# Kernel tuning notes

Measured on AMD Instinct MI355X. Metric: run time of the kernel, lower is better.

Reference implementation:

```python
import jax, jax.numpy as jnp
import numpy as np

B, L, A, D = 4, 512, 8, 256
H = 256  # hidden_dim
O = 256  # output_dim


def setup_inputs() -> dict:
    key = jax.random.key(0)
    ks = jax.random.split(key, 12)
    s = 0.05
    return {
        "x": jax.random.normal(ks[0], (B, L, A, D), dtype=jnp.float32),
        "conv_w": jax.random.normal(ks[1], (H, D), dtype=jnp.float32) * s,
        "conv_b": jax.random.normal(ks[2], (H,), dtype=jnp.float32) * s,
        "theta_w": jax.random.normal(ks[3], (H, H), dtype=jnp.float32) * s,
        "theta_b": jax.random.normal(ks[4], (H,), dtype=jnp.float32) * s,
        "phi_w": jax.random.normal(ks[5], (H, H), dtype=jnp.float32) * s,
        "phi_b": jax.random.normal(ks[6], (H,), dtype=jnp.float32) * s,
        "g_w": jax.random.normal(ks[7], (H, H), dtype=jnp.float32) * s,
        "g_b": jax.random.normal(ks[8], (H,), dtype=jnp.float32) * s,
        "f_w": jax.random.normal(ks[9], (O, H), dtype=jnp.float32) * s,
        "f_b": jax.random.normal(ks[10], (O,), dtype=jnp.float32) * s,
    }


def reference(x, conv_w, conv_b, theta_w, theta_b, phi_w, phi_b, g_w, g_b, f_w, f_b):
    batch, length, n_agents, _ = x.shape
    # residual: identity (input_dim == output_dim, stride 1)
    res = x
    # conv with kernel (1,1): pointwise projection over channel dim
    h = jnp.einsum('blad,hd->blah', x, conv_w) + conv_b  # [B,L,A,H]
    N = length * n_agents
    h = h.reshape(batch, N, H)
    theta = jnp.einsum('bnh,kh->bnk', h, theta_w) + theta_b  # [B,N,H]
    phi = jnp.einsum('bnh,kh->bnk', h, phi_w) + phi_b        # [B,N,H]
    g = jnp.einsum('bnh,kh->bnk', h, g_w) + g_b              # [B,N,H]
    scores = jnp.einsum('bnk,bmk->bnm', theta, phi) / jnp.sqrt(jnp.asarray(H, theta.dtype))
    y = jax.nn.softmax(scores, axis=2)                       # [B,N,N]
    z = jnp.einsum('bnm,bmk->bnk', y, g) / jnp.sqrt(jnp.asarray(N, y.dtype))
    out = jnp.einsum('bnk,ok->bno', z, f_w) + f_b            # [B,N,O]
    out = out.reshape(batch, length, n_agents, O)
    return out + res
```

## Files before the change

### kernel.cpp

```cpp
#include <hip/hip_runtime.h>

typedef unsigned short u16;
typedef __bf16 bf16x8 __attribute__((ext_vector_type(8)));
typedef float f32x4 __attribute__((ext_vector_type(4)));
typedef float f32x16 __attribute__((ext_vector_type(16)));
typedef float float4v __attribute__((ext_vector_type(4)));
typedef unsigned short u16x8 __attribute__((ext_vector_type(8)));
typedef unsigned short u16x4 __attribute__((ext_vector_type(4)));

#define MFMA16(a, b, c) __builtin_amdgcn_mfma_f32_16x16x32_bf16(a, b, c, 0, 0, 0)
#define MFMA32(a, b, c) __builtin_amdgcn_mfma_f32_32x32x16_bf16(a, b, c, 0, 0, 0)

__device__ __forceinline__ u16 f2bf(float f) {
  union { float f; unsigned u; } v; v.f = f;
  unsigned r = v.u + 0x7fffu + ((v.u >> 16) & 1u);
  return (u16)(r >> 16);
}

__device__ __forceinline__ void gload16(const void* g, void* l) {
  __builtin_amdgcn_global_load_lds(
      (__attribute__((address_space(1))) void*)g,
      (__attribute__((address_space(3))) void*)l, 16, 0, 0);
}


__global__ __launch_bounds__(256) void convert_k(
    const float* __restrict__ x, const float* __restrict__ cw,
    const float* __restrict__ tw, const float* __restrict__ pw,
    const float* __restrict__ gw, const float* __restrict__ fw,
    const float* __restrict__ tb, const float* __restrict__ pb,
    const float* __restrict__ gb,
    u16* __restrict__ xb, u16* __restrict__ cwb, u16* __restrict__ wcat,
    u16* __restrict__ fwb, float* __restrict__ bcat) {
  const int idx = blockIdx.x * 256 + threadIdx.x;
  const float* src;
  u16* dst;
  int off;
  if (idx < 1048576)      { src = x;  dst = xb;            off = idx; }
  else if (idx < 1064960) { src = cw; dst = cwb;           off = idx - 1048576; }
  else if (idx < 1081344) { src = tw; dst = wcat;          off = idx - 1064960; }
  else if (idx < 1097728) { src = pw; dst = wcat + 65536;  off = idx - 1081344; }
  else if (idx < 1114112) { src = gw; dst = wcat + 131072; off = idx - 1097728; }
  else if (idx < 1130496) { src = fw; dst = fwb;           off = idx - 1114112; }
  else if (idx < 1130688) {
    int j = (idx - 1130496) * 4;
#pragma unroll
    for (int i = 0; i < 4; ++i) {
      int k = j + i;
      bcat[k] = (k < 256) ? tb[k] : (k < 512) ? pb[k - 256] : gb[k - 512];
    }
    return;
  } else return;
  float4v v = *(const float4v*)(src + (size_t)off * 4);
  u16x4 o;
#pragma unroll
  for (int i = 0; i < 4; ++i) o[i] = f2bf(v[i]);
  *(u16x4*)(dst + (size_t)off * 4) = o;
}

template <int OM>
__global__ __launch_bounds__(256) void gemm_bt(
    const u16* __restrict__ A, const u16* __restrict__ W,
    const float* __restrict__ bias, void* __restrict__ Cout,
    const float* __restrict__ res, int K, int ldc) {
  __shared__ u16 As[8192];
  __shared__ u16 Bs[8192];
  const int t = threadIdx.x;
  const int lane = t & 63, w = t >> 6;
  const int brow = blockIdx.x * 128, bcol = blockIdx.y * 128;
  const int wr = (w >> 1) * 64, wc = (w & 1) * 64;
  f32x4 acc[4][4];
#pragma unroll
  for (int i = 0; i < 4; ++i)
#pragma unroll
    for (int j = 0; j < 4; ++j)
#pragma unroll
      for (int r = 0; r < 4; ++r) acc[i][j][r] = 0.0f;

  const int sr = t >> 3, sc8 = (t & 7) * 8;
  const u16* gA = A + (size_t)(brow + sr) * K + sc8;
  const u16* gW = W + (size_t)(bcol + sr) * K + sc8;

  for (int kt = 0; kt < K; kt += 64) {
#pragma unroll
    for (int c = 0; c < 4; ++c) {
      gload16(gA + (size_t)c * 32 * K + kt, &As[c * 2048 + t * 8]);
      gload16(gW + (size_t)c * 32 * K + kt, &Bs[c * 2048 + t * 8]);
    }
    __syncthreads();
#pragma unroll
    for (int kk = 0; kk < 2; ++kk) {
      const int ko = kk * 32 + (lane >> 4) * 8;
      bf16x8 af[4], bfr[4];
#pragma unroll
      for (int i = 0; i < 4; ++i)
        af[i] = *(const bf16x8*)(&As[(wr + i * 16 + (lane & 15)) * 64 + ko]);
#pragma unroll
      for (int j = 0; j < 4; ++j)
        bfr[j] = *(const bf16x8*)(&Bs[(wc + j * 16 + (lane & 15)) * 64 + ko]);
#pragma unroll
      for (int i = 0; i < 4; ++i)
#pragma unroll
        for (int j = 0; j < 4; ++j)
          acc[i][j] = MFMA16(af[i], bfr[j], acc[i][j]);
    }
    __syncthreads();
  }

  const int r0 = (lane >> 4) * 4, c0 = lane & 15;
#pragma unroll
  for (int i = 0; i < 4; ++i)
#pragma unroll
    for (int j = 0; j < 4; ++j) {
      const int col = bcol + wc + j * 16 + c0;
      const float bv = bias[col];
#pragma unroll
      for (int r = 0; r < 4; ++r) {
        const size_t o = (size_t)(brow + wr + i * 16 + r0 + r) * ldc + col;
        if (OM == 0) ((u16*)Cout)[o] = f2bf(acc[i][j][r] + bv);
        else         ((float*)Cout)[o] = acc[i][j][r] + bv + res[o];
      }
    }
}

__global__ __launch_bounds__(256) void transpose_g_k(
    const u16* __restrict__ tpg, u16* __restrict__ gT) {
  __shared__ u16 T[64][65];
  const int t = threadIdx.x;
  const int bm = (blockIdx.x & 63) * 64;
  const int bk = ((blockIdx.x >> 6) & 3) * 64;
  const int b = blockIdx.x >> 8;
  const int r = t >> 3, c8 = (t & 7) * 8;
#pragma unroll
  for (int ch = 0; ch < 2; ++ch) {
    u16x8 v = *(const u16x8*)(tpg + (size_t)(b * 4096 + bm + r + ch * 32) * 768 + 512 + bk + c8);
#pragma unroll
    for (int j = 0; j < 8; ++j) T[r + ch * 32][c8 + j] = v[j];
  }
  __syncthreads();
#pragma unroll
  for (int ch = 0; ch < 2; ++ch) {
    u16x8 o;
#pragma unroll
    for (int j = 0; j < 8; ++j) o[j] = T[c8 + j][r + ch * 32];
    *(u16x8*)(gT + (size_t)(b * 256 + bk + r + ch * 32) * 4096 + bm + c8) = o;
  }
}

__global__ __launch_bounds__(256, 1) void flash_kernel(
    const u16* __restrict__ tpg, const u16* __restrict__ gT,
    float* __restrict__ Zp, float* __restrict__ Lp) {
  __shared__ u16 Kl[2][64 * 256];
  __shared__ u16 Vl[2][256 * 64];
  __shared__ u16 Pl[4][2048];

  const int t = threadIdx.x;
  const int lane = t & 63;
  const int w = t >> 6;
  const int l31 = lane & 31;
  const int hi = lane >> 5;

  const int bid = blockIdx.x;
  const int b = bid >> 6;
  const int qt = (bid & 63) >> 1;
  const int half = bid & 1;
  const int q0 = qt * 128 + w * 32;
  const int kv0 = half * 2048;

  bf16x8 q[16];
  {
    const u16* qp = tpg + (size_t)(b * 4096 + q0 + l31) * 768 + hi * 8;
#pragma unroll
    for (int kk = 0; kk < 16; ++kk) q[kk] = *(const bf16x8*)(qp + kk * 16);
  }

  f32x16 zacc[8];
#pragma unroll
  for (int i = 0; i < 8; ++i)
#pragma unroll
    for (int j = 0; j < 16; ++j) zacc[i][j] = 0.0f;
  float ell[16];
#pragma unroll
  for (int i = 0; i < 16; ++i) ell[i] = 0.0f;

  const int ks_r = t >> 5, ks_c = t & 31;
  const int vs_r = t >> 3, vs_c = t & 7;

  auto stage = [&](int tile, int bi) {
    const size_t krow0 = (size_t)(b * 4096 + kv0 + tile * 64);
#pragma unroll
    for (int ch = 0; ch < 8; ++ch) {
      int r = ch * 8 + ks_r;
      int csw = (ks_c ^ (r & 31)) * 8;
      gload16(tpg + (krow0 + r) * 768 + 256 + csw, &Kl[bi][ch * 2048 + t * 8]);
    }
    const size_t vbase = (size_t)b * 256 * 4096 + kv0 + tile * 64;
#pragma unroll
    for (int ch = 0; ch < 8; ++ch) {
      int n = ch * 32 + vs_r;
      int csw = (vs_c ^ (n & 7)) * 8;
      gload16(gT + vbase + (size_t)n * 4096 + csw, &Vl[bi][ch * 2048 + t * 8]);
    }
  };

  stage(0, 0);
  __syncthreads();

  for (int tile = 0; tile < 32; ++tile) {
    const int cur = tile & 1;
    if (tile + 1 < 32) stage(tile + 1, cur ^ 1);

    f32x16 s0a, s0b, s1a, s1b;
#pragma unroll
    for (int j = 0; j < 16; ++j) { s0a[j] = 0.f; s0b[j] = 0.f; s1a[j] = 0.f; s1b[j] = 0.f; }
    const u16* kb = &Kl[cur][0];
#pragma unroll
    for (int kk = 0; kk < 16; kk += 2) {
      int cA = kk * 2 + hi, cB = (kk + 1) * 2 + hi;
      bf16x8 b0a = *(const bf16x8*)(kb + l31 * 256 + ((cA ^ l31) * 8));
      bf16x8 b1a = *(const bf16x8*)(kb + (32 + l31) * 256 + ((cA ^ l31) * 8));
      bf16x8 b0b = *(const bf16x8*)(kb + l31 * 256 + ((cB ^ l31) * 8));
      bf16x8 b1b = *(const bf16x8*)(kb + (32 + l31) * 256 + ((cB ^ l31) * 8));
      s0a = MFMA32(q[kk], b0a, s0a);
      s1a = MFMA32(q[kk], b1a, s1a);
      s0b = MFMA32(q[kk + 1], b0b, s0b);
      s1b = MFMA32(q[kk + 1], b1b, s1b);
    }

    u16* pw = &Pl[w][0];
#pragma unroll
    for (int g = 0; g < 16; ++g) {
      int r = (g & 3) + 8 * (g >> 2) + 4 * hi;
      float p0 = __expf((s0a[g] + s0b[g]) * 0.0625f);
      float p1 = __expf((s1a[g] + s1b[g]) * 0.0625f);
      ell[g] += p0 + p1;
      int col0 = l31, col1 = 32 + l31;
      pw[r * 64 + (((col0 >> 3) ^ (r & 7)) * 8) + (col0 & 7)] = f2bf(p0);
      pw[r * 64 + (((col1 >> 3) ^ (r & 7)) * 8) + (col1 & 7)] = f2bf(p1);
    }

    const u16* vb = &Vl[cur][0];
#pragma unroll
    for (int kk = 0; kk < 4; ++kk) {
      int c16 = kk * 2 + hi;
      bf16x8 pa = *(const bf16x8*)(pw + l31 * 64 + ((c16 ^ (l31 & 7)) * 8));
#pragma unroll
      for (int nt = 0; nt < 8; ++nt) {
        int n = nt * 32 + l31;
        bf16x8 vv = *(const bf16x8*)(vb + n * 64 + ((c16 ^ (n & 7)) * 8));
        zacc[nt] = MFMA32(pa, vv, zacc[nt]);
      }
    }
    __syncthreads();
  }

#pragma unroll
  for (int g = 0; g < 16; ++g) {
    float e = ell[g];
#pragma unroll
    for (int m = 1; m < 32; m <<= 1) e += __shfl_xor(e, m, 64);
    ell[g] = e;
  }

  const size_t zbase = (size_t)half * (16384u * 256u) + (size_t)(b * 4096 + q0) * 256;
#pragma unroll
  for (int g = 0; g < 16; ++g) {
    int r = (g & 3) + 8 * (g >> 2) + 4 * hi;
#pragma unroll
    for (int nt = 0; nt < 8; ++nt)
      Zp[zbase + (size_t)r * 256 + nt * 32 + l31] = zacc[nt][g];
  }
  if (l31 == 0) {
#pragma unroll
    for (int g = 0; g < 16; ++g) {
      int r = (g & 3) + 8 * (g >> 2) + 4 * hi;
      Lp[half * 16384 + b * 4096 + q0 + r] = ell[g];
    }
  }
}

__global__ __launch_bounds__(256) void merge_k(
    const float* __restrict__ Zp, const float* __restrict__ Lp, u16* __restrict__ zb) {
  const int idx = blockIdx.x * 256 + threadIdx.x;
  const int m = idx >> 5;
  const int c = (idx & 31) * 8;
  const float inv = 1.0f / ((Lp[m] + Lp[16384 + m]) * 64.0f);
  const float4v a0 = *(const float4v*)(Zp + (size_t)m * 256 + c);
  const float4v a1 = *(const float4v*)(Zp + (size_t)m * 256 + c + 4);
  const float4v b0 = *(const float4v*)(Zp + 4194304 + (size_t)m * 256 + c);
  const float4v b1 = *(const float4v*)(Zp + 4194304 + (size_t)m * 256 + c + 4);
  u16x8 o;
#pragma unroll
  for (int j = 0; j < 4; ++j) o[j] = f2bf((a0[j] + b0[j]) * inv);
#pragma unroll
  for (int j = 0; j < 4; ++j) o[4 + j] = f2bf((a1[j] + b1[j]) * inv);
  *(u16x8*)(zb + (size_t)m * 256 + c) = o;
}

extern "C" void kernel_launch(void* const* d_in, const int* in_sizes, int n_in,
                              void* d_out, int out_size, void* d_ws, size_t ws_size,
                              hipStream_t stream) {
  const float* x  = (const float*)d_in[0];
  const float* cw = (const float*)d_in[1];
  const float* cb = (const float*)d_in[2];
  const float* tw = (const float*)d_in[3];
  const float* tb = (const float*)d_in[4];
  const float* pw = (const float*)d_in[5];
  const float* pb = (const float*)d_in[6];
  const float* gw = (const float*)d_in[7];
  const float* gb = (const float*)d_in[8];
  const float* fw = (const float*)d_in[9];
  const float* fb = (const float*)d_in[10];

  char* ws = (char*)d_ws;
  u16*   tpg  = (u16*)(ws);
  u16*   gT   = (u16*)(ws + 25165824);
  u16*   zb   = (u16*)(ws + 25165824);
  u16*   xb   = (u16*)(ws + 33554432);
  u16*   hb   = (u16*)(ws + 41943040);
  float* Zp   = (float*)(ws + 33554432);
  float* Lp   = (float*)(ws + 67108864);
  u16*   cwb  = (u16*)(ws + 67239936);
  u16*   wcat = (u16*)(ws + 67371008);
  u16*   fwb  = (u16*)(ws + 67764224);
  float* bcat = (float*)(ws + 67895296);

  convert_k<<<4417, 256, 0, stream>>>(x, cw, tw, pw, gw, fw, tb, pb, gb,
                                      xb, cwb, wcat, fwb, bcat);
  gemm_bt<0><<<dim3(128, 2), 256, 0, stream>>>(xb, cwb, cb, (void*)hb, nullptr, 256, 256);
  gemm_bt<0><<<dim3(128, 6), 256, 0, stream>>>(hb, wcat, bcat, (void*)tpg, nullptr, 256, 768);
  transpose_g_k<<<1024, 256, 0, stream>>>(tpg, gT);
  flash_kernel<<<256, 256, 0, stream>>>(tpg, gT, Zp, Lp);
  merge_k<<<2048, 256, 0, stream>>>(Zp, Lp, zb);
  gemm_bt<1><<<dim3(128, 2), 256, 0, stream>>>(zb, fwb, fb, d_out, x, 256, 256);
}
```

Baseline: 250.9 us.

## Restructure flash attention: transposed S, register P via permlane, 4-way KV split

Computes S transposed (K as the A operand) so the softmax probabilities can be packed to bf16 with v_cvt_pk and reshuffled with v_permlane32_swap directly into MFMA A-operand registers. This drops the LDS round-trip for P. KV tiles shrink to 32 rows and the KV range is split four ways across 512 blocks, with launch bounds allowing 2 blocks per CU to raise occupancy. Partial Z is stored as bf16 to halve merge traffic, and the partial row sums go in the output buffer as scratch. The costs are extra merge reads, bf16 rounding of the partials, and reliance on d_out being overwritten afterwards.

After: 215.2 us. 14.2% less time.

```diff
diff --git a/kernel.cpp b/kernel.cpp
--- a/kernel.cpp
+++ b/kernel.cpp
@@ -23,6 +23,14 @@
       (__attribute__((address_space(3))) void*)l, 16, 0, 0);
 }
 
+__device__ __forceinline__ unsigned cvtpk(float lo, float hi) {
+  unsigned r;
+  asm("v_cvt_pk_bf16_f32 %0, %1, %2" : "=v"(r) : "v"(lo), "v"(hi));
+  return r;
+}
+__device__ __forceinline__ void plswap(unsigned& a, unsigned& b) {
+  asm volatile("v_permlane32_swap_b32 %0, %1" : "+v"(a), "+v"(b));
+}
 
 __global__ __launch_bounds__(256) void convert_k(
     const float* __restrict__ x, const float* __restrict__ cw,
@@ -147,31 +155,27 @@
   }
 }
 
-__global__ __launch_bounds__(256, 1) void flash_kernel(
+__global__ __launch_bounds__(256, 2) void flash2(
     const u16* __restrict__ tpg, const u16* __restrict__ gT,
-    float* __restrict__ Zp, float* __restrict__ Lp) {
-  __shared__ u16 Kl[2][64 * 256];
-  __shared__ u16 Vl[2][256 * 64];
-  __shared__ u16 Pl[4][2048];
+    u16* __restrict__ Zp, float* __restrict__ Lp) {
+  __shared__ u16 Kl[2][32 * 256];
+  __shared__ u16 Vl[2][256 * 32];
 
   const int t = threadIdx.x;
-  const int lane = t & 63;
-  const int w = t >> 6;
-  const int l31 = lane & 31;
-  const int hi = lane >> 5;
-
+  const int lane = t & 63, w = t >> 6;
+  const int l31 = lane & 31, hi = lane >> 5;
   const int bid = blockIdx.x;
-  const int b = bid >> 6;
-  const int qt = (bid & 63) >> 1;
-  const int half = bid & 1;
+  const int b = bid >> 7;
+  const int quarter = (bid >> 5) & 3;
+  const int qt = bid & 31;
   const int q0 = qt * 128 + w * 32;
-  const int kv0 = half * 2048;
+  const int kv0 = quarter * 1024;
 
   bf16x8 q[16];
   {
     const u16* qp = tpg + (size_t)(b * 4096 + q0 + l31) * 768 + hi * 8;
 #pragma unroll
-    for (int kk = 0; kk < 16; ++kk) q[kk] = *(const bf16x8*)(qp + kk * 16);
+    for (int ks = 0; ks < 16; ++ks) q[ks] = *(const bf16x8*)(qp + ks * 16);
   }
 
   f32x16 zacc[8];
@@ -179,27 +183,23 @@
   for (int i = 0; i < 8; ++i)
 #pragma unroll
     for (int j = 0; j < 16; ++j) zacc[i][j] = 0.0f;
-  float ell[16];
-#pragma unroll
-  for (int i = 0; i < 16; ++i) ell[i] = 0.0f;
-
-  const int ks_r = t >> 5, ks_c = t & 31;
-  const int vs_r = t >> 3, vs_c = t & 7;
+  float ell = 0.0f;
+
+  const int ksr = t >> 5, ksc = t & 31;
 
   auto stage = [&](int tile, int bi) {
-    const size_t krow0 = (size_t)(b * 4096 + kv0 + tile * 64);
-#pragma unroll
-    for (int ch = 0; ch < 8; ++ch) {
-      int r = ch * 8 + ks_r;
-      int csw = (ks_c ^ (r & 31)) * 8;
-      gload16(tpg + (krow0 + r) * 768 + 256 + csw, &Kl[bi][ch * 2048 + t * 8]);
-    }
-    const size_t vbase = (size_t)b * 256 * 4096 + kv0 + tile * 64;
-#pragma unroll
-    for (int ch = 0; ch < 8; ++ch) {
-      int n = ch * 32 + vs_r;
-      int csw = (vs_c ^ (n & 7)) * 8;
-      gload16(gT + vbase + (size_t)n * 4096 + csw, &Vl[bi][ch * 2048 + t * 8]);
+    const size_t krow0 = (size_t)(b * 4096 + kv0 + tile * 32);
+#pragma unroll
+    for (int ch = 0; ch < 4; ++ch) {
+      int r = ch * 8 + ksr;
+      gload16(tpg + (krow0 + r) * 768 + 256 + ((ksc ^ r) * 8), &Kl[bi][ch * 2048 + t * 8]);
+    }
+#pragma unroll
+    for (int ch = 0; ch < 4; ++ch) {
+      int u = ch * 256 + t;
+      int r = u >> 2, c16 = u & 3;
+      gload16(gT + (size_t)(b * 256 + r) * 4096 + kv0 + tile * 32 + ((c16 ^ ((r >> 1) & 3)) * 8),
+              &Vl[bi][u * 8]);
     }
   };
 
@@ -210,90 +210,82 @@
     const int cur = tile & 1;
     if (tile + 1 < 32) stage(tile + 1, cur ^ 1);
 
-    f32x16 s0a, s0b, s1a, s1b;
-#pragma unroll
-    for (int j = 0; j < 16; ++j) { s0a[j] = 0.f; s0b[j] = 0.f; s1a[j] = 0.f; s1b[j] = 0.f; }
+    f32x16 s;
+#pragma unroll
+    for (int j = 0; j < 16; ++j) s[j] = 0.0f;
     const u16* kb = &Kl[cur][0];
 #pragma unroll
-    for (int kk = 0; kk < 16; kk += 2) {
-      int cA = kk * 2 + hi, cB = (kk + 1) * 2 + hi;
-      bf16x8 b0a = *(const bf16x8*)(kb + l31 * 256 + ((cA ^ l31) * 8));
-      bf16x8 b1a = *(const bf16x8*)(kb + (32 + l31) * 256 + ((cA ^ l31) * 8));
-      bf16x8 b0b = *(const bf16x8*)(kb + l31 * 256 + ((cB ^ l31) * 8));
-      bf16x8 b1b = *(const bf16x8*)(kb + (32 + l31) * 256 + ((cB ^ l31) * 8));
-      s0a = MFMA32(q[kk], b0a, s0a);
-      s1a = MFMA32(q[kk], b1a, s1a);
-      s0b = MFMA32(q[kk + 1], b0b, s0b);
-      s1b = MFMA32(q[kk + 1], b1b, s1b);
-    }
-
-    u16* pw = &Pl[w][0];
-#pragma unroll
-    for (int g = 0; g < 16; ++g) {
-      int r = (g & 3) + 8 * (g >> 2) + 4 * hi;
-      float p0 = __expf((s0a[g] + s0b[g]) * 0.0625f);
-      float p1 = __expf((s1a[g] + s1b[g]) * 0.0625f);
-      ell[g] += p0 + p1;
-      int col0 = l31, col1 = 32 + l31;
-      pw[r * 64 + (((col0 >> 3) ^ (r & 7)) * 8) + (col0 & 7)] = f2bf(p0);
-      pw[r * 64 + (((col1 >> 3) ^ (r & 7)) * 8) + (col1 & 7)] = f2bf(p1);
+    for (int ks = 0; ks < 16; ++ks) {
+      bf16x8 kf = *(const bf16x8*)(kb + l31 * 256 + (((2 * ks + hi) ^ l31) * 8));
+      s = MFMA32(kf, q[ks], s);
+    }
+
+    bf16x8 pa[2];
+#pragma unroll
+    for (int half = 0; half < 2; ++half) {
+      float p[8];
+#pragma unroll
+      for (int g = 0; g < 8; ++g) {
+        p[g] = __builtin_amdgcn_exp2f(s[half * 8 + g] * 0.09016844f);
+        ell += p[g];
+      }
+      unsigned x0 = cvtpk(p[0], p[1]), y0 = cvtpk(p[4], p[5]);
+      unsigned x1 = cvtpk(p[2], p[3]), y1 = cvtpk(p[6], p[7]);
+      plswap(x0, y0);
+      plswap(x1, y1);
+      union { unsigned u[4]; bf16x8 v; } cc;
+      cc.u[0] = x0; cc.u[1] = x1; cc.u[2] = y0; cc.u[3] = y1;
+      pa[half] = cc.v;
     }
 
     const u16* vb = &Vl[cur][0];
 #pragma unroll
-    for (int kk = 0; kk < 4; ++kk) {
-      int c16 = kk * 2 + hi;
-      bf16x8 pa = *(const bf16x8*)(pw + l31 * 64 + ((c16 ^ (l31 & 7)) * 8));
+    for (int ks2 = 0; ks2 < 2; ++ks2) {
 #pragma unroll
       for (int nt = 0; nt < 8; ++nt) {
-        int n = nt * 32 + l31;
-        bf16x8 vv = *(const bf16x8*)(vb + n * 64 + ((c16 ^ (n & 7)) * 8));
-        zacc[nt] = MFMA32(pa, vv, zacc[nt]);
+        int row = nt * 32 + l31;
+        bf16x8 vv = *(const bf16x8*)(vb + row * 32 + (((2 * ks2 + hi) ^ ((row >> 1) & 3)) * 8));
+        zacc[nt] = MFMA32(pa[ks2], vv, zacc[nt]);
       }
     }
     __syncthreads();
   }
 
-#pragma unroll
-  for (int g = 0; g < 16; ++g) {
-    float e = ell[g];
-#pragma unroll
-    for (int m = 1; m < 32; m <<= 1) e += __shfl_xor(e, m, 64);
-    ell[g] = e;
-  }
-
-  const size_t zbase = (size_t)half * (16384u * 256u) + (size_t)(b * 4096 + q0) * 256;
+  ell += __shfl_xor(ell, 32, 64);
+
 #pragma unroll
   for (int g = 0; g < 16; ++g) {
     int r = (g & 3) + 8 * (g >> 2) + 4 * hi;
-#pragma unroll
-    for (int nt = 0; nt < 8; ++nt)
-      Zp[zbase + (size_t)r * 256 + nt * 32 + l31] = zacc[nt][g];
-  }
-  if (l31 == 0) {
-#pragma unroll
-    for (int g = 0; g < 16; ++g) {
-      int r = (g & 3) + 8 * (g >> 2) + 4 * hi;
-      Lp[half * 16384 + b * 4096 + q0 + r] = ell[g];
-    }
-  }
-}
-
-__global__ __launch_bounds__(256) void merge_k(
-    const float* __restrict__ Zp, const float* __restrict__ Lp, u16* __restrict__ zb) {
+    size_t rowoff = ((size_t)(quarter * 16384 + b * 4096 + q0 + r)) * 256 + l31;
+#pragma unroll
+    for (int nt = 0; nt < 8; ++nt) Zp[rowoff + nt * 32] = f2bf(zacc[nt][g]);
+  }
+  if (lane < 32) Lp[quarter * 16384 + b * 4096 + q0 + l31] = ell;
+}
+
+__global__ __launch_bounds__(256) void merge2(
+    const u16* __restrict__ Zp, const float* __restrict__ Lp, u16* __restrict__ zb) {
   const int idx = blockIdx.x * 256 + threadIdx.x;
   const int m = idx >> 5;
   const int c = (idx & 31) * 8;
-  const float inv = 1.0f / ((Lp[m] + Lp[16384 + m]) * 64.0f);
-  const float4v a0 = *(const float4v*)(Zp + (size_t)m * 256 + c);
-  const float4v a1 = *(const float4v*)(Zp + (size_t)m * 256 + c + 4);
-  const float4v b0 = *(const float4v*)(Zp + 4194304 + (size_t)m * 256 + c);
-  const float4v b1 = *(const float4v*)(Zp + 4194304 + (size_t)m * 256 + c + 4);
+  const float l = Lp[m] + Lp[16384 + m] + Lp[32768 + m] + Lp[49152 + m];
+  const float inv = 1.0f / (l * 64.0f);
+  float acc[8];
+#pragma unroll
+  for (int j = 0; j < 8; ++j) acc[j] = 0.0f;
+#pragma unroll
+  for (int qd = 0; qd < 4; ++qd) {
+    u16x8 v = *(const u16x8*)(Zp + ((size_t)(qd * 16384) + m) * 256 + c);
+#pragma unroll
+    for (int j = 0; j < 8; ++j) {
+      union { unsigned u; float f; } cv;
+      cv.u = ((unsigned)v[j]) << 16;
+      acc[j] += cv.f;
+    }
+  }
   u16x8 o;
 #pragma unroll
-  for (int j = 0; j < 4; ++j) o[j] = f2bf((a0[j] + b0[j]) * inv);
-#pragma unroll
-  for (int j = 0; j < 4; ++j) o[4 + j] = f2bf((a1[j] + b1[j]) * inv);
+  for (int j = 0; j < 8; ++j) o[j] = f2bf(acc[j] * inv);
   *(u16x8*)(zb + (size_t)m * 256 + c) = o;
 }
 
@@ -318,19 +310,19 @@
   u16*   zb   = (u16*)(ws + 25165824);
   u16*   xb   = (u16*)(ws + 33554432);
   u16*   hb   = (u16*)(ws + 41943040);
-  float* Zp   = (float*)(ws + 33554432);
-  float* Lp   = (float*)(ws + 67108864);
+  u16*   Zp   = (u16*)(ws + 33554432);
   u16*   cwb  = (u16*)(ws + 67239936);
   u16*   wcat = (u16*)(ws + 67371008);
   u16*   fwb  = (u16*)(ws + 67764224);
   float* bcat = (float*)(ws + 67895296);
+  float* Lp   = (float*)d_out;
 
   convert_k<<<4417, 256, 0, stream>>>(x, cw, tw, pw, gw, fw, tb, pb, gb,
                                       xb, cwb, wcat, fwb, bcat);
   gemm_bt<0><<<dim3(128, 2), 256, 0, stream>>>(xb, cwb, cb, (void*)hb, nullptr, 256, 256);
   gemm_bt<0><<<dim3(128, 6), 256, 0, stream>>>(hb, wcat, bcat, (void*)tpg, nullptr, 256, 768);
   transpose_g_k<<<1024, 256, 0, stream>>>(tpg, gT);
-  flash_kernel<<<256, 256, 0, stream>>>(tpg, gT, Zp, Lp);
-  merge_k<<<2048, 256, 0, stream>>>(Zp, Lp, zb);
+  flash2<<<512, 256, 0, stream>>>(tpg, gT, Zp, Lp);
+  merge2<<<2048, 256, 0, stream>>>(Zp, Lp, zb);
   gemm_bt<1><<<dim3(128, 2), 256, 0, stream>>>(zb, fwb, fb, d_out, x, 256, 256);
 }
```
